# Kernel optimization log

Hardware: AMD Instinct MI355X
Metric: run time of the kernel (lower is better)

Reference implementation:

```python
import jax, jax.numpy as jnp
import numpy as np

B, D, H, V, T = 64, 1024, 1024, 32000, 20
SOS = 0  # word_to_idx['<SOS>']


def setup_inputs() -> dict:
    key = jax.random.key(0)
    ks = jax.random.split(key, 6)
    s = 0.02
    return {
        "latent_vector": jax.random.normal(ks[0], (B, D), jnp.float32),
        "W_proj": jax.random.normal(ks[1], (H, D), jnp.float32) * s,
        "b_proj": jnp.zeros((H,), jnp.float32),
        "emb": jax.random.normal(ks[2], (V, H), jnp.float32) * s,
        "W_ih": jax.random.normal(ks[3], (3 * H, H), jnp.float32) * s,
        "b_ih": jnp.zeros((3 * H,), jnp.float32),
        "W_hh": jax.random.normal(ks[4], (3 * H, H), jnp.float32) * s,
        "b_hh": jnp.zeros((3 * H,), jnp.float32),
        "W_out": jax.random.normal(ks[5], (V, H), jnp.float32) * s,
        "b_out": jnp.zeros((V,), jnp.float32),
    }


def _gru_cell(x, h, W_ih, b_ih, W_hh, b_hh):
    # PyTorch GRU cell gate math
    gi = x @ W_ih.T + b_ih  # [B, 3H]
    gh = h @ W_hh.T + b_hh  # [B, 3H]
    i_r, i_z, i_n = jnp.split(gi, 3, axis=-1)
    h_r, h_z, h_n = jnp.split(gh, 3, axis=-1)
    r = jax.nn.sigmoid(i_r + h_r)
    z = jax.nn.sigmoid(i_z + h_z)
    n = jnp.tanh(i_n + r * h_n)
    return (1.0 - z) * n + z * h


def reference(latent_vector, W_proj, b_proj, emb, W_ih, b_ih, W_hh, b_hh, W_out, b_out):
    batch = latent_vector.shape[0]
    h = latent_vector @ W_proj.T + b_proj  # init_hidden: [B, H]
    tok0 = jnp.full((batch,), SOS, dtype=jnp.int32)

    def step(carry, _):
        tok, h = carry
        x = emb[tok]                                  # embedding lookup [B, H]
        h = _gru_cell(x, h, W_ih, b_ih, W_hh, b_hh)   # GRU step
        logits = h @ W_out.T + b_out                  # [B, V]
        tok = jnp.argmax(logits, axis=-1).astype(jnp.int32)  # topk(1) greedy
        return (tok, h), tok

    (_, h_final), toks = jax.lax.scan(step, (tok0, h), None, length=T)
    # torch: stack(outputs, dim=1).squeeze() -> [B, T]; hidden -> [1, B, H]
    return toks.T, h_final[None, :, :]
```

## Files before the change

kernel.cpp:

```cpp
#include <hip/hip_runtime.h>
#include <stdint.h>

#define B_ 64
#define D_ 1024
#define H_ 1024
#define V_ 32000
#define T_ 20

typedef __attribute__((ext_vector_type(8))) __bf16 bf16x8;
typedef __attribute__((ext_vector_type(4))) float f32x4;

__device__ __forceinline__ uint32_t ord_of_float(float x) {
    uint32_t u = __float_as_uint(x);
    return (u & 0x80000000u) ? ~u : (u | 0x80000000u);
}

__device__ __forceinline__ unsigned long long shfl_xor_u64(unsigned long long x, int m) {
    return (unsigned long long)__shfl_xor((long long)x, m, 64);
}

__device__ __forceinline__ void split_bf16(float f, unsigned short* hi, unsigned short* lo) {
    uint32_t u = __float_as_uint(f);
    uint32_t rh = (u + 0x7FFFu + ((u >> 16) & 1u)) >> 16;
    *hi = (unsigned short)rh;
    float fl = f - __uint_as_float(rh << 16);
    uint32_t ul = __float_as_uint(fl);
    uint32_t rl = (ul + 0x7FFFu + ((ul >> 16) & 1u)) >> 16;
    *lo = (unsigned short)rl;
}

__global__ __launch_bounds__(256) void k_init_hidden(
    const float* __restrict__ latent, const float* __restrict__ Wp,
    const float* __restrict__ bp, float* __restrict__ h0)
{
    int gw = (blockIdx.x * 256 + threadIdx.x) >> 6;
    int lane = threadIdx.x & 63;
    int j = gw >> 6;
    int b = gw & 63;
    const float4* a4 = (const float4*)(latent + b * D_);
    const float4* w4 = (const float4*)(Wp + (size_t)j * D_);
    float s = 0.f;
#pragma unroll
    for (int i = 0; i < 4; i++) {
        float4 a = a4[lane + 64 * i];
        float4 w = w4[lane + 64 * i];
        s += a.x * w.x + a.y * w.y + a.z * w.z + a.w * w.w;
    }
#pragma unroll
    for (int off = 32; off; off >>= 1) s += __shfl_down(s, off, 64);
    if (lane == 0) h0[b * H_ + j] = s + bp[j];
}

#define LSTRIDE 72

__global__ __launch_bounds__(256) void k_gates_gemm(
    const float* __restrict__ emb, const int* __restrict__ tok, int use_sos,
    const float* __restrict__ hprev, const float* __restrict__ Wih,
    const float* __restrict__ Whh, float* __restrict__ gbuf)
{
    __shared__ unsigned short Ahi[64 * LSTRIDE], Alo[64 * LSTRIDE];
    __shared__ unsigned short Bhi[64 * LSTRIDE], Blo[64 * LSTRIDE];
    int tid = threadIdx.x;
    int lane = tid & 63;
    int wv = tid >> 6;
    int blk = blockIdx.x;
    int jt = blk % 48;
    int rest = blk / 48;
    int half = rest & 1;
    int ks = rest >> 1;
    int kbase = ks * 512;

    const float* W = half ? Whh : Wih;

    int srow = tid >> 2;
    int scol = (tid & 3) * 16;
    const float* arow;
    if (half == 0) {
        int xr = use_sos ? 0 : tok[srow];
        arow = emb + (size_t)xr * H_;
    } else {
        arow = hprev + srow * H_;
    }
    const float* asrc = arow + kbase + scol;
    const float* bsrc = W + (size_t)(jt * 64 + srow) * H_ + kbase + scol;

    unsigned short* ahd = Ahi + srow * LSTRIDE + scol;
    unsigned short* ald = Alo + srow * LSTRIDE + scol;
    unsigned short* bhd = Bhi + srow * LSTRIDE + scol;
    unsigned short* bld = Blo + srow * LSTRIDE + scol;

    f32x4 acc[4];
#pragma unroll
    for (int i = 0; i < 4; i++) acc[i] = (f32x4){0.f, 0.f, 0.f, 0.f};

    int arow_f = wv * 16 + (lane & 15);
    int koff = (lane >> 4) * 8;

    for (int kc = 0; kc < 512; kc += 64) {
        float4 av[4], bv[4];
#pragma unroll
        for (int i = 0; i < 4; i++) {
            av[i] = *(const float4*)(asrc + kc + 4 * i);
            bv[i] = *(const float4*)(bsrc + kc + 4 * i);
        }
        __syncthreads();
#pragma unroll
        for (int i = 0; i < 4; i++) {
            split_bf16(av[i].x, ahd + 4 * i + 0, ald + 4 * i + 0);
            split_bf16(av[i].y, ahd + 4 * i + 1, ald + 4 * i + 1);
            split_bf16(av[i].z, ahd + 4 * i + 2, ald + 4 * i + 2);
            split_bf16(av[i].w, ahd + 4 * i + 3, ald + 4 * i + 3);
            split_bf16(bv[i].x, bhd + 4 * i + 0, bld + 4 * i + 0);
            split_bf16(bv[i].y, bhd + 4 * i + 1, bld + 4 * i + 1);
            split_bf16(bv[i].z, bhd + 4 * i + 2, bld + 4 * i + 2);
            split_bf16(bv[i].w, bhd + 4 * i + 3, bld + 4 * i + 3);
        }
        __syncthreads();
        bf16x8 ah0 = *(const bf16x8*)(Ahi + arow_f * LSTRIDE + koff);
        bf16x8 ah1 = *(const bf16x8*)(Ahi + arow_f * LSTRIDE + 32 + koff);
        bf16x8 al0 = *(const bf16x8*)(Alo + arow_f * LSTRIDE + koff);
        bf16x8 al1 = *(const bf16x8*)(Alo + arow_f * LSTRIDE + 32 + koff);
#pragma unroll
        for (int tv = 0; tv < 4; tv++) {
            int brow = tv * 16 + (lane & 15);
            bf16x8 bh0 = *(const bf16x8*)(Bhi + brow * LSTRIDE + koff);
            bf16x8 bh1 = *(const bf16x8*)(Bhi + brow * LSTRIDE + 32 + koff);
            bf16x8 bl0 = *(const bf16x8*)(Blo + brow * LSTRIDE + koff);
            bf16x8 bl1 = *(const bf16x8*)(Blo + brow * LSTRIDE + 32 + koff);
            acc[tv] = __builtin_amdgcn_mfma_f32_16x16x32_bf16(ah0, bh0, acc[tv], 0, 0, 0);
            acc[tv] = __builtin_amdgcn_mfma_f32_16x16x32_bf16(ah1, bh1, acc[tv], 0, 0, 0);
            acc[tv] = __builtin_amdgcn_mfma_f32_16x16x32_bf16(al0, bh0, acc[tv], 0, 0, 0);
            acc[tv] = __builtin_amdgcn_mfma_f32_16x16x32_bf16(al1, bh1, acc[tv], 0, 0, 0);
            acc[tv] = __builtin_amdgcn_mfma_f32_16x16x32_bf16(ah0, bl0, acc[tv], 0, 0, 0);
            acc[tv] = __builtin_amdgcn_mfma_f32_16x16x32_bf16(ah1, bl1, acc[tv], 0, 0, 0);
        }
    }

    int col = lane & 15;
    int quad = lane >> 4;
    float* og = gbuf + (size_t)((ks * 2 + half) * 64) * 3072;
#pragma unroll
    for (int tv = 0; tv < 4; tv++) {
#pragma unroll
        for (int r = 0; r < 4; r++) {
            int b = wv * 16 + quad * 4 + r;
            og[(size_t)b * 3072 + jt * 64 + tv * 16 + col] = acc[tv][r];
        }
    }
}

__global__ __launch_bounds__(256) void k_gru_elem(
    const float* __restrict__ gbuf, const float* __restrict__ bih,
    const float* __restrict__ bhh, const float* __restrict__ hprev,
    float* __restrict__ hnext)
{
    int idx = blockIdx.x * 256 + threadIdx.x;
    int b = idx >> 10;
    int j = idx & 1023;
    const float* g00 = gbuf + (size_t)b * 3072;
    const float* g01 = gbuf + (size_t)(64 + b) * 3072;
    const float* g10 = gbuf + (size_t)(128 + b) * 3072;
    const float* g11 = gbuf + (size_t)(192 + b) * 3072;
    float ir = g00[j] + g10[j] + bih[j];
    float hr = g01[j] + g11[j] + bhh[j];
    float iz = g00[H_ + j] + g10[H_ + j] + bih[H_ + j];
    float hz = g01[H_ + j] + g11[H_ + j] + bhh[H_ + j];
    float in_ = g00[2 * H_ + j] + g10[2 * H_ + j] + bih[2 * H_ + j];
    float hn = g01[2 * H_ + j] + g11[2 * H_ + j] + bhh[2 * H_ + j];
    float r = 1.f / (1.f + expf(-(ir + hr)));
    float z = 1.f / (1.f + expf(-(iz + hz)));
    float n = tanhf(in_ + r * hn);
    float hp = hprev[idx];
    hnext[idx] = (1.f - z) * n + z * hp;
}

__global__ __launch_bounds__(256) void k_logits_argmax(
    const float* __restrict__ hcur, const float* __restrict__ Wout,
    const float* __restrict__ bout, unsigned long long* __restrict__ partials,
    int nblk)
{
    __shared__ unsigned short Ahi[64 * LSTRIDE], Alo[64 * LSTRIDE];
    __shared__ unsigned short Bhi[64 * LSTRIDE], Blo[64 * LSTRIDE];
    int tid = threadIdx.x;
    int lane = tid & 63;
    int wv = tid >> 6;
    int vbase = blockIdx.x * 64;

    int srow = tid >> 2;
    int scol = (tid & 3) * 16;
    const float* asrc = hcur + srow * H_ + scol;
    const float* bsrc = Wout + (size_t)(vbase + srow) * H_ + scol;
    unsigned short* ahd = Ahi + srow * LSTRIDE + scol;
    unsigned short* ald = Alo + srow * LSTRIDE + scol;
    unsigned short* bhd = Bhi + srow * LSTRIDE + scol;
    unsigned short* bld = Blo + srow * LSTRIDE + scol;

    f32x4 acc[4];
#pragma unroll
    for (int i = 0; i < 4; i++) acc[i] = (f32x4){0.f, 0.f, 0.f, 0.f};

    int arow = wv * 16 + (lane & 15);
    int koff = (lane >> 4) * 8;

    for (int kc = 0; kc < H_; kc += 64) {
        float4 av[4], bv[4];
#pragma unroll
        for (int i = 0; i < 4; i++) {
            av[i] = *(const float4*)(asrc + kc + 4 * i);
            bv[i] = *(const float4*)(bsrc + kc + 4 * i);
        }
        __syncthreads();
#pragma unroll
        for (int i = 0; i < 4; i++) {
            split_bf16(av[i].x, ahd + 4 * i + 0, ald + 4 * i + 0);
            split_bf16(av[i].y, ahd + 4 * i + 1, ald + 4 * i + 1);
            split_bf16(av[i].z, ahd + 4 * i + 2, ald + 4 * i + 2);
            split_bf16(av[i].w, ahd + 4 * i + 3, ald + 4 * i + 3);
            split_bf16(bv[i].x, bhd + 4 * i + 0, bld + 4 * i + 0);
            split_bf16(bv[i].y, bhd + 4 * i + 1, bld + 4 * i + 1);
            split_bf16(bv[i].z, bhd + 4 * i + 2, bld + 4 * i + 2);
            split_bf16(bv[i].w, bhd + 4 * i + 3, bld + 4 * i + 3);
        }
        __syncthreads();
        bf16x8 ah0 = *(const bf16x8*)(Ahi + arow * LSTRIDE + koff);
        bf16x8 ah1 = *(const bf16x8*)(Ahi + arow * LSTRIDE + 32 + koff);
        bf16x8 al0 = *(const bf16x8*)(Alo + arow * LSTRIDE + koff);
        bf16x8 al1 = *(const bf16x8*)(Alo + arow * LSTRIDE + 32 + koff);
#pragma unroll
        for (int tv = 0; tv < 4; tv++) {
            int brow = tv * 16 + (lane & 15);
            bf16x8 bh0 = *(const bf16x8*)(Bhi + brow * LSTRIDE + koff);
            bf16x8 bh1 = *(const bf16x8*)(Bhi + brow * LSTRIDE + 32 + koff);
            bf16x8 bl0 = *(const bf16x8*)(Blo + brow * LSTRIDE + koff);
            bf16x8 bl1 = *(const bf16x8*)(Blo + brow * LSTRIDE + 32 + koff);
            acc[tv] = __builtin_amdgcn_mfma_f32_16x16x32_bf16(ah0, bh0, acc[tv], 0, 0, 0);
            acc[tv] = __builtin_amdgcn_mfma_f32_16x16x32_bf16(ah1, bh1, acc[tv], 0, 0, 0);
            acc[tv] = __builtin_amdgcn_mfma_f32_16x16x32_bf16(al0, bh0, acc[tv], 0, 0, 0);
            acc[tv] = __builtin_amdgcn_mfma_f32_16x16x32_bf16(al1, bh1, acc[tv], 0, 0, 0);
            acc[tv] = __builtin_amdgcn_mfma_f32_16x16x32_bf16(ah0, bl0, acc[tv], 0, 0, 0);
            acc[tv] = __builtin_amdgcn_mfma_f32_16x16x32_bf16(ah1, bl1, acc[tv], 0, 0, 0);
        }
    }

    int col = lane & 15;
    int quad = lane >> 4;
    unsigned long long kmax[4] = {0ull, 0ull, 0ull, 0ull};
#pragma unroll
    for (int tv = 0; tv < 4; tv++) {
        int v = vbase + tv * 16 + col;
        float bo = bout[v];
#pragma unroll
        for (int r = 0; r < 4; r++) {
            float lg = acc[tv][r] + bo;
            unsigned long long key = ((unsigned long long)ord_of_float(lg) << 32)
                                   | (unsigned long long)(0x7FFFFFFFu - (uint32_t)v);
            if (key > kmax[r]) kmax[r] = key;
        }
    }
#pragma unroll
    for (int r = 0; r < 4; r++) {
        unsigned long long k = kmax[r];
#pragma unroll
        for (int off = 1; off < 16; off <<= 1) {
            unsigned long long o = shfl_xor_u64(k, off);
            if (o > k) k = o;
        }
        kmax[r] = k;
    }
    if (col == 0) {
#pragma unroll
        for (int r = 0; r < 4; r++) {
            int b = wv * 16 + quad * 4 + r;
            partials[(size_t)b * nblk + blockIdx.x] = kmax[r];
        }
    }
}

__global__ __launch_bounds__(64) void k_token(
    const unsigned long long* __restrict__ partials, int nblk,
    int* __restrict__ tok, float* __restrict__ out_tokens, int t)
{
    int b = blockIdx.x;
    int lane = threadIdx.x;
    unsigned long long k = 0ull;
    for (int i = lane; i < nblk; i += 64) {
        unsigned long long p = partials[(size_t)b * nblk + i];
        if (p > k) k = p;
    }
#pragma unroll
    for (int off = 32; off; off >>= 1) {
        unsigned long long o = shfl_xor_u64(k, off);
        if (o > k) k = o;
    }
    if (lane == 0) {
        int v = (int)(0x7FFFFFFFu - (uint32_t)(k & 0xFFFFFFFFull));
        tok[b] = v;
        out_tokens[b * T_ + t] = (float)v;
    }
}

__global__ __launch_bounds__(256) void k_copy_h(const float* __restrict__ h,
                                               float* __restrict__ out)
{
    int i = (blockIdx.x * 256 + threadIdx.x) * 4;
    *(float4*)(out + i) = *(const float4*)(h + i);
}

extern "C" void kernel_launch(void* const* d_in, const int* in_sizes, int n_in,
                              void* d_out, int out_size, void* d_ws, size_t ws_size,
                              hipStream_t stream)
{
    const float* latent = (const float*)d_in[0];
    const float* Wp     = (const float*)d_in[1];
    const float* bp     = (const float*)d_in[2];
    const float* emb    = (const float*)d_in[3];
    const float* Wih    = (const float*)d_in[4];
    const float* bih    = (const float*)d_in[5];
    const float* Whh    = (const float*)d_in[6];
    const float* bhh    = (const float*)d_in[7];
    const float* Wout   = (const float*)d_in[8];
    const float* bout   = (const float*)d_in[9];
    float* out = (float*)d_out;

    char* ws = (char*)d_ws;
    float* h0 = (float*)ws;
    float* h1 = (float*)(ws + 262144);
    int* tok  = (int*)(ws + 524288);
    unsigned long long* partials = (unsigned long long*)(ws + 525312);
    float* gbuf = (float*)(ws + 786432);
    const int NBLK = V_ / 64;

    k_init_hidden<<<16384, 256, 0, stream>>>(latent, Wp, bp, h0);

    float* hp = h0;
    float* hn = h1;
    for (int t = 0; t < T_; t++) {
        k_gates_gemm<<<192, 256, 0, stream>>>(emb, tok, t == 0 ? 1 : 0,
                                              hp, Wih, Whh, gbuf);
        k_gru_elem<<<256, 256, 0, stream>>>(gbuf, bih, bhh, hp, hn);
        k_logits_argmax<<<NBLK, 256, 0, stream>>>(hn, Wout, bout, partials, NBLK);
        k_token<<<B_, 64, 0, stream>>>(partials, NBLK, tok, out, t);
        float* tmp = hp; hp = hn; hn = tmp;
    }
    k_copy_h<<<64, 256, 0, stream>>>(hp, out + B_ * T_);
}
```

Measured before the change: 1.418 ms.

## Fuse decode loop into one persistent cooperative kernel with grid syncs

Replaces the roughly 80 per-step kernel launches with a single cooperative persistent kernel of 512 blocks that runs projection, gate GEMM, GRU update and logits/argmax in phases separated by grid.sync. The gate GEMM is split four ways along K (384 blocks) instead of two to fill more CUs, the token reduction moves into the gate phase, and the initial projection uses MFMA instead of per-warp dot products. This removes launch gaps and some small kernels, but adds grid-wide barrier cost and requires every block to be co-resident. The old multi-kernel path stays as a fallback if the cooperative launch fails.

```diff
diff --git a/kernel.cpp b/kernel.cpp
--- a/kernel.cpp
+++ b/kernel.cpp
@@ -1,5 +1,8 @@
 #include <hip/hip_runtime.h>
+#include <hip/hip_cooperative_groups.h>
 #include <stdint.h>
+
+namespace cg = cooperative_groups;
 
 #define B_ 64
 #define D_ 1024
@@ -9,6 +12,8 @@
 
 typedef __attribute__((ext_vector_type(8))) __bf16 bf16x8;
 typedef __attribute__((ext_vector_type(4))) float f32x4;
+
+#define LSTRIDE 72
 
 __device__ __forceinline__ uint32_t ord_of_float(float x) {
     uint32_t u = __float_as_uint(x);
@@ -29,6 +34,266 @@
     *lo = (unsigned short)rl;
 }
 
+__device__ __forceinline__ void gemm_kc(
+    const float* __restrict__ asrc, const float* __restrict__ bsrc,
+    unsigned short* Ahi, unsigned short* Alo,
+    unsigned short* Bhi, unsigned short* Blo,
+    int srow, int scol, int arow_f, int koff, int lane, f32x4* acc)
+{
+    float4 av[4], bv[4];
+#pragma unroll
+    for (int i = 0; i < 4; i++) {
+        av[i] = *(const float4*)(asrc + 4 * i);
+        bv[i] = *(const float4*)(bsrc + 4 * i);
+    }
+    __syncthreads();
+    unsigned short* ahd = Ahi + srow * LSTRIDE + scol;
+    unsigned short* ald = Alo + srow * LSTRIDE + scol;
+    unsigned short* bhd = Bhi + srow * LSTRIDE + scol;
+    unsigned short* bld = Blo + srow * LSTRIDE + scol;
+#pragma unroll
+    for (int i = 0; i < 4; i++) {
+        split_bf16(av[i].x, ahd + 4 * i + 0, ald + 4 * i + 0);
+        split_bf16(av[i].y, ahd + 4 * i + 1, ald + 4 * i + 1);
+        split_bf16(av[i].z, ahd + 4 * i + 2, ald + 4 * i + 2);
+        split_bf16(av[i].w, ahd + 4 * i + 3, ald + 4 * i + 3);
+        split_bf16(bv[i].x, bhd + 4 * i + 0, bld + 4 * i + 0);
+        split_bf16(bv[i].y, bhd + 4 * i + 1, bld + 4 * i + 1);
+        split_bf16(bv[i].z, bhd + 4 * i + 2, bld + 4 * i + 2);
+        split_bf16(bv[i].w, bhd + 4 * i + 3, bld + 4 * i + 3);
+    }
+    __syncthreads();
+    bf16x8 ah0 = *(const bf16x8*)(Ahi + arow_f * LSTRIDE + koff);
+    bf16x8 ah1 = *(const bf16x8*)(Ahi + arow_f * LSTRIDE + 32 + koff);
+    bf16x8 al0 = *(const bf16x8*)(Alo + arow_f * LSTRIDE + koff);
+    bf16x8 al1 = *(const bf16x8*)(Alo + arow_f * LSTRIDE + 32 + koff);
+#pragma unroll
+    for (int tv = 0; tv < 4; tv++) {
+        int brow = tv * 16 + (lane & 15);
+        bf16x8 bh0 = *(const bf16x8*)(Bhi + brow * LSTRIDE + koff);
+        bf16x8 bh1 = *(const bf16x8*)(Bhi + brow * LSTRIDE + 32 + koff);
+        bf16x8 bl0 = *(const bf16x8*)(Blo + brow * LSTRIDE + koff);
+        bf16x8 bl1 = *(const bf16x8*)(Blo + brow * LSTRIDE + 32 + koff);
+        acc[tv] = __builtin_amdgcn_mfma_f32_16x16x32_bf16(ah0, bh0, acc[tv], 0, 0, 0);
+        acc[tv] = __builtin_amdgcn_mfma_f32_16x16x32_bf16(ah1, bh1, acc[tv], 0, 0, 0);
+        acc[tv] = __builtin_amdgcn_mfma_f32_16x16x32_bf16(al0, bh0, acc[tv], 0, 0, 0);
+        acc[tv] = __builtin_amdgcn_mfma_f32_16x16x32_bf16(al1, bh1, acc[tv], 0, 0, 0);
+        acc[tv] = __builtin_amdgcn_mfma_f32_16x16x32_bf16(ah0, bl0, acc[tv], 0, 0, 0);
+        acc[tv] = __builtin_amdgcn_mfma_f32_16x16x32_bf16(ah1, bl1, acc[tv], 0, 0, 0);
+    }
+}
+
+__global__ __launch_bounds__(256, 2) void k_persist(
+    const float* __restrict__ latent, const float* __restrict__ Wp,
+    const float* __restrict__ bp, const float* __restrict__ emb,
+    const float* __restrict__ Wih, const float* __restrict__ bih,
+    const float* __restrict__ Whh, const float* __restrict__ bhh,
+    const float* __restrict__ Wout, const float* __restrict__ bout,
+    float* __restrict__ out, char* __restrict__ ws)
+{
+    cg::grid_group grid = cg::this_grid();
+
+    __shared__ unsigned short Ahi[64 * LSTRIDE], Alo[64 * LSTRIDE];
+    __shared__ unsigned short Bhi[64 * LSTRIDE], Blo[64 * LSTRIDE];
+    __shared__ int tokLds[64];
+    __shared__ unsigned long long redLds[64];
+
+    float* hb0 = (float*)ws;
+    float* hb1 = (float*)(ws + 262144);
+    unsigned long long* partials = (unsigned long long*)(ws + 524288);
+    float* gbuf = (float*)(ws + 786432);
+
+    int tid = threadIdx.x;
+    int lane = tid & 63;
+    int wv = tid >> 6;
+    int bx = blockIdx.x;
+    int srow = tid >> 2;
+    int scol = (tid & 3) * 16;
+    int arow_f = wv * 16 + (lane & 15);
+    int koff = (lane >> 4) * 8;
+    int col = lane & 15;
+    int quad = lane >> 4;
+
+    if (bx < 16) {
+        int jt = bx;
+        const float* asrc = latent + srow * D_ + scol;
+        const float* bsrc = Wp + (size_t)(jt * 64 + srow) * D_ + scol;
+        f32x4 acc[4];
+#pragma unroll
+        for (int i = 0; i < 4; i++) acc[i] = (f32x4){0.f, 0.f, 0.f, 0.f};
+        for (int kc = 0; kc < D_; kc += 64)
+            gemm_kc(asrc + kc, bsrc + kc, Ahi, Alo, Bhi, Blo,
+                    srow, scol, arow_f, koff, lane, acc);
+#pragma unroll
+        for (int tv = 0; tv < 4; tv++) {
+            int j = jt * 64 + tv * 16 + col;
+#pragma unroll
+            for (int r = 0; r < 4; r++) {
+                int b = wv * 16 + quad * 4 + r;
+                hb0[b * H_ + j] = acc[tv][r] + bp[j];
+            }
+        }
+    }
+    grid.sync();
+
+    for (int t = 0; t < T_; t++) {
+        const float* hprev = (t & 1) ? hb1 : hb0;
+        float* hnext = (t & 1) ? hb0 : hb1;
+
+        if (bx < 384) {
+            int jt = bx % 48;
+            int rest = bx / 48;
+            int half = rest & 1;
+            int ks = rest >> 1;
+            int kbase = ks * 256;
+
+            if (half == 0) {
+                if (t == 0) {
+                    if (tid < 64) tokLds[tid] = 0;
+                } else {
+                    int b = tid & 63, chunk = tid >> 6;
+                    unsigned long long k = 0ull;
+                    int i0 = chunk * 125;
+                    for (int i = i0; i < i0 + 125; i++) {
+                        unsigned long long p = partials[(size_t)i * 64 + b];
+                        if (p > k) k = p;
+                    }
+                    if (tid < 64) redLds[tid] = 0ull;
+                    __syncthreads();
+                    atomicMax(&redLds[b], k);
+                    __syncthreads();
+                    if (tid < 64)
+                        tokLds[tid] = (int)(0x7FFFFFFFu -
+                                      (uint32_t)(redLds[tid] & 0xFFFFFFFFull));
+                }
+            }
+            __syncthreads();
+            if (bx == 0 && t > 0 && tid < 64)
+                out[tid * T_ + (t - 1)] = (float)tokLds[tid];
+
+            const float* asrc;
+            if (half == 0)
+                asrc = emb + (size_t)tokLds[srow] * H_ + kbase + scol;
+            else
+                asrc = hprev + srow * H_ + kbase + scol;
+            const float* W = half ? Whh : Wih;
+            const float* bsrc = W + (size_t)(jt * 64 + srow) * H_ + kbase + scol;
+
+            f32x4 acc[4];
+#pragma unroll
+            for (int i = 0; i < 4; i++) acc[i] = (f32x4){0.f, 0.f, 0.f, 0.f};
+            for (int kc = 0; kc < 256; kc += 64)
+                gemm_kc(asrc + kc, bsrc + kc, Ahi, Alo, Bhi, Blo,
+                        srow, scol, arow_f, koff, lane, acc);
+
+            float* og = gbuf + (size_t)((ks * 2 + half) * 64) * 3072;
+#pragma unroll
+            for (int tv = 0; tv < 4; tv++) {
+#pragma unroll
+                for (int r = 0; r < 4; r++) {
+                    int b = wv * 16 + quad * 4 + r;
+                    og[(size_t)b * 3072 + jt * 64 + tv * 16 + col] = acc[tv][r];
+                }
+            }
+        }
+        grid.sync();
+
+        {
+            int gid = bx * 256 + tid;
+            if (gid < 65536) {
+                int b = gid >> 10, j = gid & 1023;
+                float ir = bih[j], iz = bih[H_ + j], in_ = bih[2 * H_ + j];
+                float hr = bhh[j], hz = bhh[H_ + j], hn = bhh[2 * H_ + j];
+#pragma unroll
+                for (int ks = 0; ks < 4; ks++) {
+                    const float* gi = gbuf + (size_t)((ks * 2 + 0) * 64 + b) * 3072;
+                    const float* gh = gbuf + (size_t)((ks * 2 + 1) * 64 + b) * 3072;
+                    ir += gi[j];          hr += gh[j];
+                    iz += gi[H_ + j];     hz += gh[H_ + j];
+                    in_ += gi[2 * H_ + j]; hn += gh[2 * H_ + j];
+                }
+                float r = 1.f / (1.f + expf(-(ir + hr)));
+                float z = 1.f / (1.f + expf(-(iz + hz)));
+                float n = tanhf(in_ + r * hn);
+                hnext[gid] = (1.f - z) * n + z * hprev[gid];
+            }
+        }
+        grid.sync();
+
+        if (bx < 500) {
+            const float* asrc = hnext + srow * H_ + scol;
+            const float* bsrc = Wout + (size_t)(bx * 64 + srow) * H_ + scol;
+            f32x4 acc[4];
+#pragma unroll
+            for (int i = 0; i < 4; i++) acc[i] = (f32x4){0.f, 0.f, 0.f, 0.f};
+            for (int kc = 0; kc < H_; kc += 64)
+                gemm_kc(asrc + kc, bsrc + kc, Ahi, Alo, Bhi, Blo,
+                        srow, scol, arow_f, koff, lane, acc);
+
+            unsigned long long kmax[4] = {0ull, 0ull, 0ull, 0ull};
+#pragma unroll
+            for (int tv = 0; tv < 4; tv++) {
+                int v = bx * 64 + tv * 16 + col;
+                float bo = bout[v];
+#pragma unroll
+                for (int r = 0; r < 4; r++) {
+                    float lg = acc[tv][r] + bo;
+                    unsigned long long key =
+                        ((unsigned long long)ord_of_float(lg) << 32)
+                        | (unsigned long long)(0x7FFFFFFFu - (uint32_t)v);
+                    if (key > kmax[r]) kmax[r] = key;
+                }
+            }
+#pragma unroll
+            for (int r = 0; r < 4; r++) {
+                unsigned long long k = kmax[r];
+#pragma unroll
+                for (int off = 1; off < 16; off <<= 1) {
+                    unsigned long long o = shfl_xor_u64(k, off);
+                    if (o > k) k = o;
+                }
+                kmax[r] = k;
+            }
+            if (col == 0) {
+#pragma unroll
+                for (int r = 0; r < 4; r++) {
+                    int b = wv * 16 + quad * 4 + r;
+                    partials[(size_t)bx * 64 + b] = kmax[r];
+                }
+            }
+        }
+        grid.sync();
+    }
+
+    if (bx < 64) {
+        int b = bx;
+        unsigned long long k = 0ull;
+        for (int i = tid; i < 500; i += 256) {
+            unsigned long long p = partials[(size_t)i * 64 + b];
+            if (p > k) k = p;
+        }
+#pragma unroll
+        for (int off = 32; off; off >>= 1) {
+            unsigned long long o = shfl_xor_u64(k, off);
+            if (o > k) k = o;
+        }
+        if (lane == 0) redLds[wv] = k;
+        __syncthreads();
+        if (tid == 0) {
+            unsigned long long km = redLds[0];
+            for (int i = 1; i < 4; i++) if (redLds[i] > km) km = redLds[i];
+            out[b * T_ + 19] =
+                (float)(int)(0x7FFFFFFFu - (uint32_t)(km & 0xFFFFFFFFull));
+        }
+    }
+    {
+        int gid = bx * 256 + tid;
+        if (gid < 16384) {
+            ((float4*)(out + B_ * T_))[gid] = ((const float4*)hb0)[gid];
+        }
+    }
+}
+
 __global__ __launch_bounds__(256) void k_init_hidden(
     const float* __restrict__ latent, const float* __restrict__ Wp,
     const float* __restrict__ bp, float* __restrict__ h0)
@@ -50,8 +315,6 @@
     for (int off = 32; off; off >>= 1) s += __shfl_down(s, off, 64);
     if (lane == 0) h0[b * H_ + j] = s + bp[j];
 }
-
-#define LSTRIDE 72
 
 __global__ __launch_bounds__(256) void k_gates_gemm(
     const float* __restrict__ emb, const int* __restrict__ tok, int use_sos,
@@ -69,9 +332,7 @@
     int half = rest & 1;
     int ks = rest >> 1;
     int kbase = ks * 512;
-
     const float* W = half ? Whh : Wih;
-
     int srow = tid >> 2;
     int scol = (tid & 3) * 16;
     const float* arow;
@@ -83,70 +344,24 @@
     }
     const float* asrc = arow + kbase + scol;
     const float* bsrc = W + (size_t)(jt * 64 + srow) * H_ + kbase + scol;
-
-    unsigned short* ahd = Ahi + srow * LSTRIDE + scol;
-    unsigned short* ald = Alo + srow * LSTRIDE + scol;
-    unsigned short* bhd = Bhi + srow * LSTRIDE + scol;
-    unsigned short* bld = Blo + srow * LSTRIDE + scol;
-
     f32x4 acc[4];
 #pragma unroll
     for (int i = 0; i < 4; i++) acc[i] = (f32x4){0.f, 0.f, 0.f, 0.f};
-
     int arow_f = wv * 16 + (lane & 15);
     int koff = (lane >> 4) * 8;
-
-    for (int kc = 0; kc < 512; kc += 64) {
-        float4 av[4], bv[4];
-#pragma unroll
-        for (int i = 0; i < 4; i++) {
-            av[i] = *(const float4*)(asrc + kc + 4 * i);
-            bv[i] = *(const float4*)(bsrc + kc + 4 * i);
-        }
-        __syncthreads();
-#pragma unroll
-        for (int i = 0; i < 4; i++) {
-            split_bf16(av[i].x, ahd + 4 * i + 0, ald + 4 * i + 0);
-            split_bf16(av[i].y, ahd + 4 * i + 1, ald + 4 * i + 1);
-            split_bf16(av[i].z, ahd + 4 * i + 2, ald + 4 * i + 2);
-            split_bf16(av[i].w, ahd + 4 * i + 3, ald + 4 * i + 3);
-            split_bf16(bv[i].x, bhd + 4 * i + 0, bld + 4 * i + 0);
-            split_bf16(bv[i].y, bhd + 4 * i + 1, bld + 4 * i + 1);
-            split_bf16(bv[i].z, bhd + 4 * i + 2, bld + 4 * i + 2);
-            split_bf16(bv[i].w, bhd + 4 * i + 3, bld + 4 * i + 3);
-        }
-        __syncthreads();
-        bf16x8 ah0 = *(const bf16x8*)(Ahi + arow_f * LSTRIDE + koff);
-        bf16x8 ah1 = *(const bf16x8*)(Ahi + arow_f * LSTRIDE + 32 + koff);
-        bf16x8 al0 = *(const bf16x8*)(Alo + arow_f * LSTRIDE + koff);
-        bf16x8 al1 = *(const bf16x8*)(Alo + arow_f * LSTRIDE + 32 + koff);
-#pragma unroll
-        for (int tv = 0; tv < 4; tv++) {
-            int brow = tv * 16 + (lane & 15);
-            bf16x8 bh0 = *(const bf16x8*)(Bhi + brow * LSTRIDE + koff);
-            bf16x8 bh1 = *(const bf16x8*)(Bhi + brow * LSTRIDE + 32 + koff);
-            bf16x8 bl0 = *(const bf16x8*)(Blo + brow * LSTRIDE + koff);
-            bf16x8 bl1 = *(const bf16x8*)(Blo + brow * LSTRIDE + 32 + koff);
-            acc[tv] = __builtin_amdgcn_mfma_f32_16x16x32_bf16(ah0, bh0, acc[tv], 0, 0, 0);
-            acc[tv] = __builtin_amdgcn_mfma_f32_16x16x32_bf16(ah1, bh1, acc[tv], 0, 0, 0);
-            acc[tv] = __builtin_amdgcn_mfma_f32_16x16x32_bf16(al0, bh0, acc[tv], 0, 0, 0);
-            acc[tv] = __builtin_amdgcn_mfma_f32_16x16x32_bf16(al1, bh1, acc[tv], 0, 0, 0);
-            acc[tv] = __builtin_amdgcn_mfma_f32_16x16x32_bf16(ah0, bl0, acc[tv], 0, 0, 0);
-            acc[tv] = __builtin_amdgcn_mfma_f32_16x16x32_bf16(ah1, bl1, acc[tv], 0, 0, 0);
-        }
-    }
-
+    for (int kc = 0; kc < 512; kc += 64)
+        gemm_kc(asrc + kc, bsrc + kc, Ahi, Alo, Bhi, Blo,
+                srow, scol, arow_f, koff, lane, acc);
     int col = lane & 15;
     int quad = lane >> 4;
     float* og = gbuf + (size_t)((ks * 2 + half) * 64) * 3072;
 #pragma unroll
-    for (int tv = 0; tv < 4; tv++) {
+    for (int tv = 0; tv < 4; tv++)
 #pragma unroll
         for (int r = 0; r < 4; r++) {
             int b = wv * 16 + quad * 4 + r;
             og[(size_t)b * 3072 + jt * 64 + tv * 16 + col] = acc[tv][r];
         }
-    }
 }
 
 __global__ __launch_bounds__(256) void k_gru_elem(
@@ -170,8 +385,7 @@
     float r = 1.f / (1.f + expf(-(ir + hr)));
     float z = 1.f / (1.f + expf(-(iz + hz)));
     float n = tanhf(in_ + r * hn);
-    float hp = hprev[idx];
-    hnext[idx] = (1.f - z) * n + z * hp;
+    hnext[idx] = (1.f - z) * n + z * hprev[idx];
 }
 
 __global__ __launch_bounds__(256) void k_logits_argmax(
@@ -185,63 +399,18 @@
     int lane = tid & 63;
     int wv = tid >> 6;
     int vbase = blockIdx.x * 64;
-
     int srow = tid >> 2;
     int scol = (tid & 3) * 16;
     const float* asrc = hcur + srow * H_ + scol;
     const float* bsrc = Wout + (size_t)(vbase + srow) * H_ + scol;
-    unsigned short* ahd = Ahi + srow * LSTRIDE + scol;
-    unsigned short* ald = Alo + srow * LSTRIDE + scol;
-    unsigned short* bhd = Bhi + srow * LSTRIDE + scol;
-    unsigned short* bld = Blo + srow * LSTRIDE + scol;
-
     f32x4 acc[4];
 #pragma unroll
     for (int i = 0; i < 4; i++) acc[i] = (f32x4){0.f, 0.f, 0.f, 0.f};
-
-    int arow = wv * 16 + (lane & 15);
+    int arow_f = wv * 16 + (lane & 15);
     int koff = (lane >> 4) * 8;
-
-    for (int kc = 0; kc < H_; kc += 64) {
-        float4 av[4], bv[4];
-#pragma unroll
-        for (int i = 0; i < 4; i++) {
-            av[i] = *(const float4*)(asrc + kc + 4 * i);
-            bv[i] = *(const float4*)(bsrc + kc + 4 * i);
-        }
-        __syncthreads();
-#pragma unroll
-        for (int i = 0; i < 4; i++) {
-            split_bf16(av[i].x, ahd + 4 * i + 0, ald + 4 * i + 0);
-            split_bf16(av[i].y, ahd + 4 * i + 1, ald + 4 * i + 1);
-            split_bf16(av[i].z, ahd + 4 * i + 2, ald + 4 * i + 2);
-            split_bf16(av[i].w, ahd + 4 * i + 3, ald + 4 * i + 3);
-            split_bf16(bv[i].x, bhd + 4 * i + 0, bld + 4 * i + 0);
-            split_bf16(bv[i].y, bhd + 4 * i + 1, bld + 4 * i + 1);
-            split_bf16(bv[i].z, bhd + 4 * i + 2, bld + 4 * i + 2);
-            split_bf16(bv[i].w, bhd + 4 * i + 3, bld + 4 * i + 3);
-        }
-        __syncthreads();
-        bf16x8 ah0 = *(const bf16x8*)(Ahi + arow * LSTRIDE + koff);
-        bf16x8 ah1 = *(const bf16x8*)(Ahi + arow * LSTRIDE + 32 + koff);
-        bf16x8 al0 = *(const bf16x8*)(Alo + arow * LSTRIDE + koff);
-        bf16x8 al1 = *(const bf16x8*)(Alo + arow * LSTRIDE + 32 + koff);
-#pragma unroll
-        for (int tv = 0; tv < 4; tv++) {
-            int brow = tv * 16 + (lane & 15);
-            bf16x8 bh0 = *(const bf16x8*)(Bhi + brow * LSTRIDE + koff);
-            bf16x8 bh1 = *(const bf16x8*)(Bhi + brow * LSTRIDE + 32 + koff);
-            bf16x8 bl0 = *(const bf16x8*)(Blo + brow * LSTRIDE + koff);
-            bf16x8 bl1 = *(const bf16x8*)(Blo + brow * LSTRIDE + 32 + koff);
-            acc[tv] = __builtin_amdgcn_mfma_f32_16x16x32_bf16(ah0, bh0, acc[tv], 0, 0, 0);
-            acc[tv] = __builtin_amdgcn_mfma_f32_16x16x32_bf16(ah1, bh1, acc[tv], 0, 0, 0);
-            acc[tv] = __builtin_amdgcn_mfma_f32_16x16x32_bf16(al0, bh0, acc[tv], 0, 0, 0);
-            acc[tv] = __builtin_amdgcn_mfma_f32_16x16x32_bf16(al1, bh1, acc[tv], 0, 0, 0);
-            acc[tv] = __builtin_amdgcn_mfma_f32_16x16x32_bf16(ah0, bl0, acc[tv], 0, 0, 0);
-            acc[tv] = __builtin_amdgcn_mfma_f32_16x16x32_bf16(ah1, bl1, acc[tv], 0, 0, 0);
-        }
-    }
-
+    for (int kc = 0; kc < H_; kc += 64)
+        gemm_kc(asrc + kc, bsrc + kc, Ahi, Alo, Bhi, Blo,
+                srow, scol, arow_f, koff, lane, acc);
     int col = lane & 15;
     int quad = lane >> 4;
     unsigned long long kmax[4] = {0ull, 0ull, 0ull, 0ull};
@@ -267,13 +436,12 @@
         }
         kmax[r] = k;
     }
-    if (col == 0) {
+    if (col == 0)
 #pragma unroll
         for (int r = 0; r < 4; r++) {
             int b = wv * 16 + quad * 4 + r;
             partials[(size_t)b * nblk + blockIdx.x] = kmax[r];
         }
-    }
 }
 
 __global__ __launch_bounds__(64) void k_token(
@@ -321,17 +489,26 @@
     const float* Wout   = (const float*)d_in[8];
     const float* bout   = (const float*)d_in[9];
     float* out = (float*)d_out;
-
     char* ws = (char*)d_ws;
+
+    void* args[] = {
+        (void*)&latent, (void*)&Wp, (void*)&bp, (void*)&emb,
+        (void*)&Wih, (void*)&bih, (void*)&Whh, (void*)&bhh,
+        (void*)&Wout, (void*)&bout, (void*)&out, (void*)&ws
+    };
+    hipError_t e = hipLaunchCooperativeKernel((const void*)k_persist,
+                                              dim3(512), dim3(256),
+                                              args, 0, stream);
+    if (e == hipSuccess) return;
+
     float* h0 = (float*)ws;
     float* h1 = (float*)(ws + 262144);
     int* tok  = (int*)(ws + 524288);
     unsigned long long* partials = (unsigned long long*)(ws + 525312);
-    float* gbuf = (float*)(ws + 786432);
+    float* gbuf = (float*)(ws + 8388608);
     const int NBLK = V_ / 64;
 
     k_init_hidden<<<16384, 256, 0, stream>>>(latent, Wp, bp, h0);
-
     float* hp = h0;
     float* hn = h1;
     for (int t = 0; t < T_; t++) {
```

Measured after the change: 4.766 ms. +236.2%, slower.
